# Optimization experiments

Measured on AMD Instinct MI355X. Metric: run time of the kernel, lower is better.

The kernel has to match this reference:

```python
import jax, jax.numpy as jnp
import numpy as np

N_NODES = 40000
N_EDGES = 320000
IN_C = 256
OUT_C = 256
K = 5


def setup_inputs() -> dict:
    key = jax.random.key(0)
    k1, k2, k3, k4, k5 = jax.random.split(key, 5)
    x = jax.random.normal(k1, (N_NODES, IN_C), dtype=jnp.float32)
    edge_index = jax.random.randint(k2, (2, N_EDGES), 0, N_NODES, dtype=jnp.int64)
    edge_weight = jax.random.uniform(k3, (N_EDGES,), dtype=jnp.float32)
    # parameters: uniform(-stdv, stdv) with stdv = 1/sqrt(in_channels * K)
    stdv = 1.0 / np.sqrt(IN_C * K)
    weight = jax.random.uniform(k4, (K, IN_C, OUT_C), dtype=jnp.float32,
                                minval=-stdv, maxval=stdv)
    bias = jax.random.uniform(k5, (OUT_C,), dtype=jnp.float32,
                              minval=-stdv, maxval=stdv)
    return {"x": x, "edge_index": edge_index, "edge_weight": edge_weight,
            "weight": weight, "bias": bias}


def reference(x, edge_index, edge_weight, weight, bias):
    row, col = edge_index[0], edge_index[1]
    num_nodes = x.shape[0]
    k_order = weight.shape[0]

    # remove_self_loops: mask out row==col edges (static-shape equivalent)
    keep = (row != col)
    ew = jnp.where(keep, edge_weight, 0.0)

    # degree over rows (counting only non-self-loop edges), D^{-1/2}
    deg = jax.ops.segment_sum(keep.astype(x.dtype), row, num_segments=num_nodes)
    deg_inv_sqrt = jnp.where(deg > 0, jax.lax.rsqrt(jnp.maximum(deg, 1.0)), 0.0)

    # scaled Laplacian edge values: -d_r^{-1/2} * w * d_c^{-1/2}
    lap = -deg_inv_sqrt[row] * ew * deg_inv_sqrt[col]

    def spmm(v):  # [N, C] -> [N, C] : scatter-add of lap-weighted gathered rows
        return jax.ops.segment_sum(lap[:, None] * v[col], row, num_segments=num_nodes)

    # Chebyshev recursion: T0 = x, T1 = L x, T_k = 2 L T_{k-1} - T_{k-2}
    tx0 = x
    out = tx0 @ weight[0]
    if k_order > 1:
        tx1 = spmm(x)
        out = out + tx1 @ weight[1]
        for k in range(2, k_order):
            tx2 = 2.0 * spmm(tx1) - tx0
            out = out + tx2 @ weight[k]
            tx0, tx1 = tx1, tx2
    return out + bias
```

## Files before the change

kernel.cpp:

```cpp
#include <hip/hip_runtime.h>

#define NN 40000
#define NE 320000
#define C 256
#define KORD 5
#define KT 1280

typedef __attribute__((ext_vector_type(8))) short short8;
typedef __attribute__((ext_vector_type(4))) float floatx4;
typedef unsigned short bf16_t;

__device__ __forceinline__ bf16_t f2bf(float f) {
    union { float f; unsigned u; } v; v.f = f;
    unsigned r = v.u + 0x7fffu + ((v.u >> 16) & 1u);
    return (bf16_t)(r >> 16);
}
__device__ __forceinline__ float bf2f(bf16_t h) {
    union { unsigned u; float f; } v; v.u = ((unsigned)h) << 16;
    return v.f;
}

#define GLL16(gsrc, ldst)                                                        \
    __builtin_amdgcn_global_load_lds(                                            \
        (const __attribute__((address_space(1))) void*)(gsrc),                   \
        (__attribute__((address_space(3))) void*)(ldst), 16, 0, 0)


__global__ void count_kernel(const int* __restrict__ ei,
                             int* __restrict__ deg_keep,
                             int* __restrict__ cnt_all) {
    int e = blockIdx.x * 256 + threadIdx.x;
    if (e >= NE) return;
    int r = ei[e];
    int c = ei[NE + e];
    atomicAdd(&cnt_all[r], 1);
    if (r != c) atomicAdd(&deg_keep[r], 1);
}

__global__ void dis_kernel(const int* __restrict__ deg, float* __restrict__ dis) {
    int n = blockIdx.x * 256 + threadIdx.x;
    if (n >= NN) return;
    int d = deg[n];
    dis[n] = (d > 0) ? rsqrtf((float)d) : 0.0f;
}

__global__ void scan1_kernel(const int* __restrict__ cnt,
                             int* __restrict__ incl,
                             int* __restrict__ bsum) {
    __shared__ int s[256];
    int t = threadIdx.x;
    int idx = blockIdx.x * 256 + t;
    int v = (idx < NN) ? cnt[idx] : 0;
    s[t] = v;
    __syncthreads();
    for (int off = 1; off < 256; off <<= 1) {
        int add = (t >= off) ? s[t - off] : 0;
        __syncthreads();
        s[t] += add;
        __syncthreads();
    }
    if (idx < NN) incl[idx] = s[t];
    if (t == 255) bsum[blockIdx.x] = s[255];
}

__global__ void scan2_kernel(int* __restrict__ bsum, int nb) {
    __shared__ int s[256];
    int t = threadIdx.x;
    int v = (t < nb) ? bsum[t] : 0;
    s[t] = v;
    __syncthreads();
    for (int off = 1; off < 256; off <<= 1) {
        int add = (t >= off) ? s[t - off] : 0;
        __syncthreads();
        s[t] += add;
        __syncthreads();
    }
    if (t < nb) bsum[t] = s[t] - v;
}

__global__ void scan3_kernel(const int* __restrict__ cnt,
                             const int* __restrict__ incl,
                             const int* __restrict__ bexcl,
                             int* __restrict__ row_ptr,
                             int* __restrict__ cursor) {
    int idx = blockIdx.x * 256 + threadIdx.x;
    if (idx == 0) row_ptr[NN] = NE;
    if (idx >= NN) return;
    int rp = incl[idx] - cnt[idx] + bexcl[blockIdx.x];
    row_ptr[idx] = rp;
    cursor[idx]  = rp;
}

__global__ void fill_kernel(const int* __restrict__ ei,
                            const float* __restrict__ ew,
                            const float* __restrict__ dis,
                            int* __restrict__ cursor,
                            int* __restrict__ csr_col,
                            float* __restrict__ csr_val) {
    int e = blockIdx.x * 256 + threadIdx.x;
    if (e >= NE) return;
    int r = ei[e];
    int c = ei[NE + e];
    int pos = atomicAdd(&cursor[r], 1);
    float w = (r != c) ? ew[e] : 0.0f;
    csr_col[pos] = c;
    csr_val[pos] = -dis[r] * w * dis[c];
}

__global__ void convx_kernel(const float* __restrict__ x, bf16_t* __restrict__ abf) {
    int i = blockIdx.x * 256 + threadIdx.x;
    if (i >= NN * 64) return;
    int n = i >> 6, cg = i & 63;
    float4 f = *(const float4*)&x[(size_t)n * C + cg * 4];
    ushort4 h;
    h.x = f2bf(f.x); h.y = f2bf(f.y); h.z = f2bf(f.z); h.w = f2bf(f.w);
    *(ushort4*)&abf[(size_t)n * KT + cg * 4] = h;
}

__global__ void wt_kernel(const float* __restrict__ W, bf16_t* __restrict__ WT) {
    int t = blockIdx.x * 256 + threadIdx.x;
    if (t >= 256 * KT) return;
    int n = t & 255, kt = t >> 8;
    WT[(size_t)n * KT + kt] = f2bf(W[(size_t)kt * 256 + n]);
}

__global__ __launch_bounds__(256)
void spmm_kernel(const bf16_t* __restrict__ Vb,
                 const bf16_t* __restrict__ subb,
                 const int* __restrict__ row_ptr,
                 const int* __restrict__ csr_col,
                 const float* __restrict__ csr_val,
                 bf16_t* __restrict__ outb,
                 float alpha, int use_sub) {
    int wave = __builtin_amdgcn_readfirstlane(threadIdx.x >> 6);
    int lane = threadIdx.x & 63;
    int n = blockIdx.x * 4 + wave;
    int j0 = row_ptr[n];
    int j1 = row_ptr[n + 1];
    int cb = lane * 4;
    float a0 = 0.f, a1 = 0.f, a2 = 0.f, a3 = 0.f;
    int j = j0;
    for (; j + 8 <= j1; j += 8) {
        int cc[8]; float ww[8]; ushort4 vv[8];
#pragma unroll
        for (int u = 0; u < 8; ++u) { cc[u] = csr_col[j + u]; ww[u] = csr_val[j + u]; }
#pragma unroll
        for (int u = 0; u < 8; ++u) vv[u] = *(const ushort4*)&Vb[(size_t)cc[u] * KT + cb];
#pragma unroll
        for (int u = 0; u < 8; ++u) {
            a0 += ww[u] * bf2f(vv[u].x); a1 += ww[u] * bf2f(vv[u].y);
            a2 += ww[u] * bf2f(vv[u].z); a3 += ww[u] * bf2f(vv[u].w);
        }
    }
    for (; j + 4 <= j1; j += 4) {
        int cc[4]; float ww[4]; ushort4 vv[4];
#pragma unroll
        for (int u = 0; u < 4; ++u) { cc[u] = csr_col[j + u]; ww[u] = csr_val[j + u]; }
#pragma unroll
        for (int u = 0; u < 4; ++u) vv[u] = *(const ushort4*)&Vb[(size_t)cc[u] * KT + cb];
#pragma unroll
        for (int u = 0; u < 4; ++u) {
            a0 += ww[u] * bf2f(vv[u].x); a1 += ww[u] * bf2f(vv[u].y);
            a2 += ww[u] * bf2f(vv[u].z); a3 += ww[u] * bf2f(vv[u].w);
        }
    }
    for (; j < j1; ++j) {
        int   col = csr_col[j];
        float w   = csr_val[j];
        ushort4 v = *(const ushort4*)&Vb[(size_t)col * KT + cb];
        a0 += w * bf2f(v.x); a1 += w * bf2f(v.y);
        a2 += w * bf2f(v.z); a3 += w * bf2f(v.w);
    }
    float r0, r1, r2, r3;
    if (use_sub) {
        ushort4 s = *(const ushort4*)&subb[(size_t)n * KT + cb];
        r0 = alpha * a0 - bf2f(s.x);
        r1 = alpha * a1 - bf2f(s.y);
        r2 = alpha * a2 - bf2f(s.z);
        r3 = alpha * a3 - bf2f(s.w);
    } else {
        r0 = alpha * a0; r1 = alpha * a1; r2 = alpha * a2; r3 = alpha * a3;
    }
    ushort4 h;
    h.x = f2bf(r0); h.y = f2bf(r1); h.z = f2bf(r2); h.w = f2bf(r3);
    *(ushort4*)&outb[(size_t)n * KT + cb] = h;
}

__global__ __launch_bounds__(256, 2)
void gemm_mfma(const bf16_t* __restrict__ Abf,
               const bf16_t* __restrict__ WT,
               const float* __restrict__ bias,
               float* __restrict__ out) {
    __shared__ bf16_t smem[3][12288];
    int tid = threadIdx.x;
    int w = tid >> 6, lane = tid & 63;
    int m0 = blockIdx.x * 64;
    int n0 = blockIdx.y * 128;
    int wm = w & 1, wn = w >> 1;
    int quad = lane >> 4, l16 = lane & 15, l7 = l16 & 7;

    const bf16_t* srcbase[6];
#pragma unroll
    for (int j = 0; j < 6; ++j) {
        int gi = (w * 6 + j) * 64 + lane;
        int isB = gi >= 512;
        int t  = isB ? gi - 512 : gi;
        int row = t >> 3;
        int pg = t & 7;
        int g  = pg ^ (row & 7);
        srcbase[j] = (isB ? WT + (size_t)(n0 + row) * KT
                          : Abf + (size_t)(m0 + row) * KT) + g * 8;
    }

    int arowb = wm * 32 + l16;
    int browb = wn * 64 + l16;

    floatx4 acc[2][4] = {};

    const int NT = KT / 64;

#pragma unroll
    for (int j = 0; j < 6; ++j)
        GLL16(srcbase[j] + 0 * 64, &smem[0][(w * 6 + j) * 512]);
#pragma unroll
    for (int j = 0; j < 6; ++j)
        GLL16(srcbase[j] + 1 * 64, &smem[1][(w * 6 + j) * 512]);

    int bufc = 0;
    for (int t = 0; t < NT; ++t) {
        if (t < NT - 1) {
            asm volatile("s_waitcnt vmcnt(6)" ::: "memory");
        } else {
            asm volatile("s_waitcnt vmcnt(0)" ::: "memory");
        }
        __builtin_amdgcn_sched_barrier(0);
        __builtin_amdgcn_s_barrier();

        if (t + 2 < NT) {
            int bnext = bufc + 2; if (bnext >= 3) bnext -= 3;
#pragma unroll
            for (int j = 0; j < 6; ++j)
                GLL16(srcbase[j] + (t + 2) * 64, &smem[bnext][(w * 6 + j) * 512]);
        }

        const bf16_t* sb = smem[bufc];
#pragma unroll
        for (int c = 0; c < 2; ++c) {
            int gp   = (c * 4 + quad) ^ l7;
            int aoff = (arowb * 8 + gp) * 8;
            int boff = 4096 + (browb * 8 + gp) * 8;
            short8 af[2], bfr[4];
#pragma unroll
            for (int mt = 0; mt < 2; ++mt) af[mt]  = *(const short8*)&sb[aoff + mt * 1024];
#pragma unroll
            for (int nt = 0; nt < 4; ++nt) bfr[nt] = *(const short8*)&sb[boff + nt * 1024];
#pragma unroll
            for (int mt = 0; mt < 2; ++mt)
#pragma unroll
                for (int nt = 0; nt < 4; ++nt)
                    acc[mt][nt] = __builtin_amdgcn_mfma_f32_16x16x32_bf16(
                        af[mt], bfr[nt], acc[mt][nt], 0, 0, 0);
        }

        bufc += 1; if (bufc == 3) bufc = 0;
    }

#pragma unroll
    for (int nt = 0; nt < 4; ++nt) {
        int n = n0 + wn * 64 + nt * 16 + l16;
        float bv = bias[n];
#pragma unroll
        for (int mt = 0; mt < 2; ++mt) {
            int mbase = m0 + wm * 32 + mt * 16 + quad * 4;
#pragma unroll
            for (int r = 0; r < 4; ++r)
                out[(size_t)(mbase + r) * C + n] = acc[mt][nt][r] + bv;
        }
    }
}


extern "C" void kernel_launch(void* const* d_in, const int* in_sizes, int n_in,
                              void* d_out, int out_size, void* d_ws, size_t ws_size,
                              hipStream_t stream) {
    const float* x    = (const float*)d_in[0];
    const int*   ei   = (const int*)d_in[1];
    const float* ew   = (const float*)d_in[2];
    const float* W    = (const float*)d_in[3];
    const float* bias = (const float*)d_in[4];
    float* out = (float*)d_out;

    char* p = (char*)d_ws;
    auto carve = [&](size_t bytes) {
        char* q = p;
        p += (bytes + 255) & ~(size_t)255;
        return q;
    };
    int*    deg     = (int*)   carve(NN * 4);
    int*    cnt     = (int*)   carve(NN * 4);
    int*    incl    = (int*)   carve(NN * 4);
    int*    bsum    = (int*)   carve(256 * 4);
    int*    row_ptr = (int*)   carve((NN + 1) * 4);
    int*    cursor  = (int*)   carve(NN * 4);
    int*    csr_col = (int*)   carve(NE * 4);
    float*  csr_val = (float*) carve(NE * 4);
    float*  dis     = (float*) carve(NN * 4);
    bf16_t* abf     = (bf16_t*)carve((size_t)NN * KT * 2);
    bf16_t* WT      = (bf16_t*)carve((size_t)C * KT * 2);
    (void)ws_size; (void)n_in; (void)in_sizes; (void)out_size;

    const int NB_E = (NE + 255) / 256;
    const int NB_N = (NN + 255) / 256;

    hipMemsetAsync(deg, 0, NN * 4, stream);
    hipMemsetAsync(cnt, 0, NN * 4, stream);

    count_kernel<<<NB_E, 256, 0, stream>>>(ei, deg, cnt);
    dis_kernel<<<NB_N, 256, 0, stream>>>(deg, dis);
    scan1_kernel<<<NB_N, 256, 0, stream>>>(cnt, incl, bsum);
    scan2_kernel<<<1, 256, 0, stream>>>(bsum, NB_N);
    scan3_kernel<<<NB_N, 256, 0, stream>>>(cnt, incl, bsum, row_ptr, cursor);
    fill_kernel<<<NB_E, 256, 0, stream>>>(ei, ew, dis, cursor, csr_col, csr_val);

    convx_kernel<<<(NN * 64 + 255) / 256, 256, 0, stream>>>(x, abf);
    wt_kernel<<<(256 * KT + 255) / 256, 256, 0, stream>>>(W, WT);

    spmm_kernel<<<NN / 4, 256, 0, stream>>>(abf + 0 * 256, nullptr, row_ptr, csr_col,
                                            csr_val, abf + 1 * 256, 1.0f, 0);
    spmm_kernel<<<NN / 4, 256, 0, stream>>>(abf + 1 * 256, abf + 0 * 256, row_ptr,
                                            csr_col, csr_val, abf + 2 * 256, 2.0f, 1);
    spmm_kernel<<<NN / 4, 256, 0, stream>>>(abf + 2 * 256, abf + 1 * 256, row_ptr,
                                            csr_col, csr_val, abf + 3 * 256, 2.0f, 1);
    spmm_kernel<<<NN / 4, 256, 0, stream>>>(abf + 3 * 256, abf + 2 * 256, row_ptr,
                                            csr_col, csr_val, abf + 4 * 256, 2.0f, 1);

    dim3 ggrid(625, 2);
    gemm_mfma<<<ggrid, 256, 0, stream>>>(abf, WT, bias, out);
}
```

Baseline: 305.8 us.

## Store Chebyshev bases in channel-sliced layout for cache-local SpMM gathers

The bf16 basis matrix changes from row-major [N, 1280] to 40 slices of [N, 32] channels (8 slices per Chebyshev order). Each SpMM block then handles one 32-channel slice for 32 nodes, so the gathered rows of one slice (2.5 MB) can stay in cache. The GEMM loader now computes slice-aware addresses and strides, and the dis computation is folded into scan3 to drop one launch. Each gather is now only 64 bytes per row with 8 lanes per node, which risks lower memory-level parallelism and redundant reads of csr_col and csr_val across the 8 slice blocks.

New measurement: 347.0 us. +13.5%, slower.

```diff
diff --git a/kernel.cpp b/kernel.cpp
--- a/kernel.cpp
+++ b/kernel.cpp
@@ -9,6 +9,8 @@
 typedef __attribute__((ext_vector_type(8))) short short8;
 typedef __attribute__((ext_vector_type(4))) float floatx4;
 typedef unsigned short bf16_t;
+
+#define SLICE_ELEMS 1280000
 
 __device__ __forceinline__ bf16_t f2bf(float f) {
     union { float f; unsigned u; } v; v.f = f;
@@ -35,13 +37,6 @@
     int c = ei[NE + e];
     atomicAdd(&cnt_all[r], 1);
     if (r != c) atomicAdd(&deg_keep[r], 1);
-}
-
-__global__ void dis_kernel(const int* __restrict__ deg, float* __restrict__ dis) {
-    int n = blockIdx.x * 256 + threadIdx.x;
-    if (n >= NN) return;
-    int d = deg[n];
-    dis[n] = (d > 0) ? rsqrtf((float)d) : 0.0f;
 }
 
 __global__ void scan1_kernel(const int* __restrict__ cnt,
@@ -81,6 +76,8 @@
 __global__ void scan3_kernel(const int* __restrict__ cnt,
                              const int* __restrict__ incl,
                              const int* __restrict__ bexcl,
+                             const int* __restrict__ deg,
+                             float* __restrict__ dis,
                              int* __restrict__ row_ptr,
                              int* __restrict__ cursor) {
     int idx = blockIdx.x * 256 + threadIdx.x;
@@ -89,6 +86,8 @@
     int rp = incl[idx] - cnt[idx] + bexcl[blockIdx.x];
     row_ptr[idx] = rp;
     cursor[idx]  = rp;
+    int d = deg[idx];
+    dis[idx] = (d > 0) ? rsqrtf((float)d) : 0.0f;
 }
 
 __global__ void fill_kernel(const int* __restrict__ ei,
@@ -107,14 +106,19 @@
     csr_val[pos] = -dis[r] * w * dis[c];
 }
 
-__global__ void convx_kernel(const float* __restrict__ x, bf16_t* __restrict__ abf) {
+__global__ void convx_kernel(const float* __restrict__ x, bf16_t* __restrict__ st) {
     int i = blockIdx.x * 256 + threadIdx.x;
-    if (i >= NN * 64) return;
-    int n = i >> 6, cg = i & 63;
-    float4 f = *(const float4*)&x[(size_t)n * C + cg * 4];
-    ushort4 h;
-    h.x = f2bf(f.x); h.y = f2bf(f.y); h.z = f2bf(f.z); h.w = f2bf(f.w);
-    *(ushort4*)&abf[(size_t)n * KT + cg * 4] = h;
+    if (i >= NN * 16) return;
+    int n = i >> 4, s = (i >> 1) & 7, h = i & 1;
+    const float* xs = &x[(size_t)n * C + s * 32 + h * 16];
+    bf16_t* o = st + (size_t)s * SLICE_ELEMS + (size_t)n * 32 + h * 16;
+#pragma unroll
+    for (int q = 0; q < 4; ++q) {
+        float4 f = *(const float4*)&xs[q * 4];
+        ushort4 hh;
+        hh.x = f2bf(f.x); hh.y = f2bf(f.y); hh.z = f2bf(f.z); hh.w = f2bf(f.w);
+        *(ushort4*)&o[q * 4] = hh;
+    }
 }
 
 __global__ void wt_kernel(const float* __restrict__ W, bf16_t* __restrict__ WT) {
@@ -125,65 +129,53 @@
 }
 
 __global__ __launch_bounds__(256)
-void spmm_kernel(const bf16_t* __restrict__ Vb,
-                 const bf16_t* __restrict__ subb,
+void spmm_kernel(bf16_t* __restrict__ st,
                  const int* __restrict__ row_ptr,
                  const int* __restrict__ csr_col,
                  const float* __restrict__ csr_val,
-                 bf16_t* __restrict__ outb,
-                 float alpha, int use_sub) {
-    int wave = __builtin_amdgcn_readfirstlane(threadIdx.x >> 6);
+                 float alpha, int kin, int kout, int ksub) {
+    int s = blockIdx.x;
+    int wave = threadIdx.x >> 6;
     int lane = threadIdx.x & 63;
-    int n = blockIdx.x * 4 + wave;
+    int r8 = lane >> 3, c8 = lane & 7;
+    int n = (blockIdx.y * 4 + wave) * 8 + r8;
     int j0 = row_ptr[n];
     int j1 = row_ptr[n + 1];
-    int cb = lane * 4;
+    const bf16_t* V = st + (size_t)(kin * 8 + s) * SLICE_ELEMS;
+    int co = c8 * 4;
     float a0 = 0.f, a1 = 0.f, a2 = 0.f, a3 = 0.f;
     int j = j0;
-    for (; j + 8 <= j1; j += 8) {
-        int cc[8]; float ww[8]; ushort4 vv[8];
-#pragma unroll
-        for (int u = 0; u < 8; ++u) { cc[u] = csr_col[j + u]; ww[u] = csr_val[j + u]; }
-#pragma unroll
-        for (int u = 0; u < 8; ++u) vv[u] = *(const ushort4*)&Vb[(size_t)cc[u] * KT + cb];
-#pragma unroll
-        for (int u = 0; u < 8; ++u) {
-            a0 += ww[u] * bf2f(vv[u].x); a1 += ww[u] * bf2f(vv[u].y);
-            a2 += ww[u] * bf2f(vv[u].z); a3 += ww[u] * bf2f(vv[u].w);
-        }
-    }
-    for (; j + 4 <= j1; j += 4) {
-        int cc[4]; float ww[4]; ushort4 vv[4];
-#pragma unroll
-        for (int u = 0; u < 4; ++u) { cc[u] = csr_col[j + u]; ww[u] = csr_val[j + u]; }
-#pragma unroll
-        for (int u = 0; u < 4; ++u) vv[u] = *(const ushort4*)&Vb[(size_t)cc[u] * KT + cb];
-#pragma unroll
-        for (int u = 0; u < 4; ++u) {
-            a0 += ww[u] * bf2f(vv[u].x); a1 += ww[u] * bf2f(vv[u].y);
-            a2 += ww[u] * bf2f(vv[u].z); a3 += ww[u] * bf2f(vv[u].w);
-        }
-    }
-    for (; j < j1; ++j) {
+    for (; j + 2 <= j1; j += 2) {
+        int   col0 = csr_col[j];     int   col1 = csr_col[j + 1];
+        float w0   = csr_val[j];     float w1   = csr_val[j + 1];
+        ushort4 v0 = *(const ushort4*)&V[(size_t)col0 * 32 + co];
+        ushort4 v1 = *(const ushort4*)&V[(size_t)col1 * 32 + co];
+        a0 += w0 * bf2f(v0.x); a1 += w0 * bf2f(v0.y);
+        a2 += w0 * bf2f(v0.z); a3 += w0 * bf2f(v0.w);
+        a0 += w1 * bf2f(v1.x); a1 += w1 * bf2f(v1.y);
+        a2 += w1 * bf2f(v1.z); a3 += w1 * bf2f(v1.w);
+    }
+    if (j < j1) {
         int   col = csr_col[j];
         float w   = csr_val[j];
-        ushort4 v = *(const ushort4*)&Vb[(size_t)col * KT + cb];
+        ushort4 v = *(const ushort4*)&V[(size_t)col * 32 + co];
         a0 += w * bf2f(v.x); a1 += w * bf2f(v.y);
         a2 += w * bf2f(v.z); a3 += w * bf2f(v.w);
     }
     float r0, r1, r2, r3;
-    if (use_sub) {
-        ushort4 s = *(const ushort4*)&subb[(size_t)n * KT + cb];
-        r0 = alpha * a0 - bf2f(s.x);
-        r1 = alpha * a1 - bf2f(s.y);
-        r2 = alpha * a2 - bf2f(s.z);
-        r3 = alpha * a3 - bf2f(s.w);
+    if (ksub >= 0) {
+        ushort4 sv = *(const ushort4*)&st[(size_t)(ksub * 8 + s) * SLICE_ELEMS
+                                          + (size_t)n * 32 + co];
+        r0 = alpha * a0 - bf2f(sv.x);
+        r1 = alpha * a1 - bf2f(sv.y);
+        r2 = alpha * a2 - bf2f(sv.z);
+        r3 = alpha * a3 - bf2f(sv.w);
     } else {
         r0 = alpha * a0; r1 = alpha * a1; r2 = alpha * a2; r3 = alpha * a3;
     }
     ushort4 h;
     h.x = f2bf(r0); h.y = f2bf(r1); h.z = f2bf(r2); h.w = f2bf(r3);
-    *(ushort4*)&outb[(size_t)n * KT + cb] = h;
+    *(ushort4*)&st[(size_t)(kout * 8 + s) * SLICE_ELEMS + (size_t)n * 32 + co] = h;
 }
 
 __global__ __launch_bounds__(256, 2)
@@ -200,6 +192,7 @@
     int quad = lane >> 4, l16 = lane & 15, l7 = l16 & 7;
 
     const bf16_t* srcbase[6];
+    size_t strd[6];
 #pragma unroll
     for (int j = 0; j < 6; ++j) {
         int gi = (w * 6 + j) * 64 + lane;
@@ -208,8 +201,14 @@
         int row = t >> 3;
         int pg = t & 7;
         int g  = pg ^ (row & 7);
-        srcbase[j] = (isB ? WT + (size_t)(n0 + row) * KT
-                          : Abf + (size_t)(m0 + row) * KT) + g * 8;
+        if (isB) {
+            srcbase[j] = WT + (size_t)(n0 + row) * KT + g * 8;
+            strd[j] = 64;
+        } else {
+            srcbase[j] = Abf + (size_t)(g >> 2) * SLICE_ELEMS
+                             + (size_t)(m0 + row) * 32 + (g & 3) * 8;
+            strd[j] = 2 * SLICE_ELEMS;
+        }
     }
 
     int arowb = wm * 32 + l16;
@@ -221,10 +220,10 @@
 
 #pragma unroll
     for (int j = 0; j < 6; ++j)
-        GLL16(srcbase[j] + 0 * 64, &smem[0][(w * 6 + j) * 512]);
+        GLL16(srcbase[j], &smem[0][(w * 6 + j) * 512]);
 #pragma unroll
     for (int j = 0; j < 6; ++j)
-        GLL16(srcbase[j] + 1 * 64, &smem[1][(w * 6 + j) * 512]);
+        GLL16(srcbase[j] + strd[j], &smem[1][(w * 6 + j) * 512]);
 
     int bufc = 0;
     for (int t = 0; t < NT; ++t) {
@@ -240,7 +239,8 @@
             int bnext = bufc + 2; if (bnext >= 3) bnext -= 3;
 #pragma unroll
             for (int j = 0; j < 6; ++j)
-                GLL16(srcbase[j] + (t + 2) * 64, &smem[bnext][(w * 6 + j) * 512]);
+                GLL16(srcbase[j] + (size_t)(t + 2) * strd[j],
+                      &smem[bnext][(w * 6 + j) * 512]);
         }
 
         const bf16_t* sb = smem[bufc];
@@ -316,23 +316,23 @@
     hipMemsetAsync(cnt, 0, NN * 4, stream);
 
     count_kernel<<<NB_E, 256, 0, stream>>>(ei, deg, cnt);
-    dis_kernel<<<NB_N, 256, 0, stream>>>(deg, dis);
     scan1_kernel<<<NB_N, 256, 0, stream>>>(cnt, incl, bsum);
     scan2_kernel<<<1, 256, 0, stream>>>(bsum, NB_N);
-    scan3_kernel<<<NB_N, 256, 0, stream>>>(cnt, incl, bsum, row_ptr, cursor);
+    scan3_kernel<<<NB_N, 256, 0, stream>>>(cnt, incl, bsum, deg, dis, row_ptr, cursor);
     fill_kernel<<<NB_E, 256, 0, stream>>>(ei, ew, dis, cursor, csr_col, csr_val);
 
-    convx_kernel<<<(NN * 64 + 255) / 256, 256, 0, stream>>>(x, abf);
+    convx_kernel<<<(NN * 16 + 255) / 256, 256, 0, stream>>>(x, abf);
     wt_kernel<<<(256 * KT + 255) / 256, 256, 0, stream>>>(W, WT);
 
-    spmm_kernel<<<NN / 4, 256, 0, stream>>>(abf + 0 * 256, nullptr, row_ptr, csr_col,
-                                            csr_val, abf + 1 * 256, 1.0f, 0);
-    spmm_kernel<<<NN / 4, 256, 0, stream>>>(abf + 1 * 256, abf + 0 * 256, row_ptr,
-                                            csr_col, csr_val, abf + 2 * 256, 2.0f, 1);
-    spmm_kernel<<<NN / 4, 256, 0, stream>>>(abf + 2 * 256, abf + 1 * 256, row_ptr,
-                                            csr_col, csr_val, abf + 3 * 256, 2.0f, 1);
-    spmm_kernel<<<NN / 4, 256, 0, stream>>>(abf + 3 * 256, abf + 2 * 256, row_ptr,
-                                            csr_col, csr_val, abf + 4 * 256, 2.0f, 1);
+    dim3 sgrid(8, NN / 32);
+    spmm_kernel<<<sgrid, 256, 0, stream>>>(abf, row_ptr, csr_col, csr_val,
+                                           1.0f, 0, 1, -1);
+    spmm_kernel<<<sgrid, 256, 0, stream>>>(abf, row_ptr, csr_col, csr_val,
+                                           2.0f, 1, 2, 0);
+    spmm_kernel<<<sgrid, 256, 0, stream>>>(abf, row_ptr, csr_col, csr_val,
+                                           2.0f, 2, 3, 1);
+    spmm_kernel<<<sgrid, 256, 0, stream>>>(abf, row_ptr, csr_col, csr_val,
+                                           2.0f, 3, 4, 2);
 
     dim3 ggrid(625, 2);
     gemm_mfma<<<ggrid, 256, 0, stream>>>(abf, WT, bias, out);
```

## Split SpMM wave into two edge halves with 16-byte gathers; fuse dis into scan3

Applied to the files above, without the earlier changes.

The SpMM kernel now has each half-wave handle alternate edges and each lane load 8 bf16 values (16 bytes) per gathered row. Each iteration processes 16 edges, with a masked tail instead of separate remainder loops, and the two halves are reduced with a cross-lane shuffle. This targets more memory-level parallelism and fewer, wider load instructions in the gather-bound loop. In exchange, half the lanes sit idle in the epilogue and padded edges reload a dummy row for low-degree nodes. Separately, the D^-1/2 computation is folded into scan3, removing one kernel launch.

Measured after the change: 316.6 us. 3.6% more time.

```diff
diff --git a/kernel.cpp b/kernel.cpp
--- a/kernel.cpp
+++ b/kernel.cpp
@@ -7,6 +7,7 @@
 #define KT 1280
 
 typedef __attribute__((ext_vector_type(8))) short short8;
+typedef __attribute__((ext_vector_type(8))) unsigned short ushort8;
 typedef __attribute__((ext_vector_type(4))) float floatx4;
 typedef unsigned short bf16_t;
 
@@ -35,13 +36,6 @@
     int c = ei[NE + e];
     atomicAdd(&cnt_all[r], 1);
     if (r != c) atomicAdd(&deg_keep[r], 1);
-}
-
-__global__ void dis_kernel(const int* __restrict__ deg, float* __restrict__ dis) {
-    int n = blockIdx.x * 256 + threadIdx.x;
-    if (n >= NN) return;
-    int d = deg[n];
-    dis[n] = (d > 0) ? rsqrtf((float)d) : 0.0f;
 }
 
 __global__ void scan1_kernel(const int* __restrict__ cnt,
@@ -81,6 +75,8 @@
 __global__ void scan3_kernel(const int* __restrict__ cnt,
                              const int* __restrict__ incl,
                              const int* __restrict__ bexcl,
+                             const int* __restrict__ deg,
+                             float* __restrict__ dis,
                              int* __restrict__ row_ptr,
                              int* __restrict__ cursor) {
     int idx = blockIdx.x * 256 + threadIdx.x;
@@ -89,6 +85,8 @@
     int rp = incl[idx] - cnt[idx] + bexcl[blockIdx.x];
     row_ptr[idx] = rp;
     cursor[idx]  = rp;
+    int d = deg[idx];
+    dis[idx] = (d > 0) ? rsqrtf((float)d) : 0.0f;
 }
 
 __global__ void fill_kernel(const int* __restrict__ ei,
@@ -137,53 +135,45 @@
     int n = blockIdx.x * 4 + wave;
     int j0 = row_ptr[n];
     int j1 = row_ptr[n + 1];
-    int cb = lane * 4;
-    float a0 = 0.f, a1 = 0.f, a2 = 0.f, a3 = 0.f;
-    int j = j0;
-    for (; j + 8 <= j1; j += 8) {
-        int cc[8]; float ww[8]; ushort4 vv[8];
-#pragma unroll
-        for (int u = 0; u < 8; ++u) { cc[u] = csr_col[j + u]; ww[u] = csr_val[j + u]; }
-#pragma unroll
-        for (int u = 0; u < 8; ++u) vv[u] = *(const ushort4*)&Vb[(size_t)cc[u] * KT + cb];
+    int half = lane >> 5;
+    int cb = (lane & 31) * 8;
+    float a[8] = {};
+    for (int jb = j0; jb < j1; jb += 16) {
+        int cc[8]; float ww[8]; ushort8 vv[8];
 #pragma unroll
         for (int u = 0; u < 8; ++u) {
-            a0 += ww[u] * bf2f(vv[u].x); a1 += ww[u] * bf2f(vv[u].y);
-            a2 += ww[u] * bf2f(vv[u].z); a3 += ww[u] * bf2f(vv[u].w);
-        }
-    }
-    for (; j + 4 <= j1; j += 4) {
-        int cc[4]; float ww[4]; ushort4 vv[4];
-#pragma unroll
-        for (int u = 0; u < 4; ++u) { cc[u] = csr_col[j + u]; ww[u] = csr_val[j + u]; }
-#pragma unroll
-        for (int u = 0; u < 4; ++u) vv[u] = *(const ushort4*)&Vb[(size_t)cc[u] * KT + cb];
-#pragma unroll
-        for (int u = 0; u < 4; ++u) {
-            a0 += ww[u] * bf2f(vv[u].x); a1 += ww[u] * bf2f(vv[u].y);
-            a2 += ww[u] * bf2f(vv[u].z); a3 += ww[u] * bf2f(vv[u].w);
-        }
-    }
-    for (; j < j1; ++j) {
-        int   col = csr_col[j];
-        float w   = csr_val[j];
-        ushort4 v = *(const ushort4*)&Vb[(size_t)col * KT + cb];
-        a0 += w * bf2f(v.x); a1 += w * bf2f(v.y);
-        a2 += w * bf2f(v.z); a3 += w * bf2f(v.w);
-    }
-    float r0, r1, r2, r3;
-    if (use_sub) {
-        ushort4 s = *(const ushort4*)&subb[(size_t)n * KT + cb];
-        r0 = alpha * a0 - bf2f(s.x);
-        r1 = alpha * a1 - bf2f(s.y);
-        r2 = alpha * a2 - bf2f(s.z);
-        r3 = alpha * a3 - bf2f(s.w);
-    } else {
-        r0 = alpha * a0; r1 = alpha * a1; r2 = alpha * a2; r3 = alpha * a3;
-    }
-    ushort4 h;
-    h.x = f2bf(r0); h.y = f2bf(r1); h.z = f2bf(r2); h.w = f2bf(r3);
-    *(ushort4*)&outb[(size_t)n * KT + cb] = h;
+            int je = jb + 2 * u + half;
+            int ok = je < j1;
+            int jc = ok ? je : j0;
+            cc[u] = csr_col[jc];
+            ww[u] = ok ? csr_val[jc] : 0.0f;
+        }
+#pragma unroll
+        for (int u = 0; u < 8; ++u)
+            vv[u] = *(const ushort8*)&Vb[(size_t)cc[u] * KT + cb];
+#pragma unroll
+        for (int u = 0; u < 8; ++u)
+#pragma unroll
+            for (int q = 0; q < 8; ++q)
+                a[q] += ww[u] * bf2f(vv[u][q]);
+    }
+#pragma unroll
+    for (int q = 0; q < 8; ++q)
+        a[q] += __shfl_xor(a[q], 32);
+    if (half == 0) {
+        ushort8 h;
+        if (use_sub) {
+            ushort8 s = *(const ushort8*)&subb[(size_t)n * KT + cb];
+#pragma unroll
+            for (int q = 0; q < 8; ++q)
+                h[q] = f2bf(alpha * a[q] - bf2f(s[q]));
+        } else {
+#pragma unroll
+            for (int q = 0; q < 8; ++q)
+                h[q] = f2bf(alpha * a[q]);
+        }
+        *(ushort8*)&outb[(size_t)n * KT + cb] = h;
+    }
 }
 
 __global__ __launch_bounds__(256, 2)
@@ -316,10 +306,9 @@
     hipMemsetAsync(cnt, 0, NN * 4, stream);
 
     count_kernel<<<NB_E, 256, 0, stream>>>(ei, deg, cnt);
-    dis_kernel<<<NB_N, 256, 0, stream>>>(deg, dis);
     scan1_kernel<<<NB_N, 256, 0, stream>>>(cnt, incl, bsum);
     scan2_kernel<<<1, 256, 0, stream>>>(bsum, NB_N);
-    scan3_kernel<<<NB_N, 256, 0, stream>>>(cnt, incl, bsum, row_ptr, cursor);
+    scan3_kernel<<<NB_N, 256, 0, stream>>>(cnt, incl, bsum, deg, dis, row_ptr, cursor);
     fill_kernel<<<NB_E, 256, 0, stream>>>(ei, ew, dis, cursor, csr_col, csr_val);
 
     convx_kernel<<<(NN * 64 + 255) / 256, 256, 0, stream>>>(x, abf);
```
